# Performance work log

Measured on AMD Instinct MI355X. Metric: run time of the kernel, lower is better.

Reference implementation:

```python
import jax, jax.numpy as jnp
import numpy as np

# Winograd F(4x4, 5x5) transform matrices (input tile 8x8)
AT_NP = np.array([
    [1.0, 1.0, 1.0, 1.0, 1.0, 8.0, 8.0, 0.0],
    [0.0, 1.0, -1.0, 2.0, -2.0, 4.0, -4.0, 0.0],
    [0.0, 1.0, 1.0, 4.0, 4.0, 2.0, 2.0, 0.0],
    [0.0, 1.0, -1.0, 8.0, -8.0, 1.0, -1.0, 1.0]], dtype=np.float32)

BT_NP = np.array([
    [1.0, 0.0, -21.0/4.0, 0.0, 21.0/4.0, 0.0, -1.0, 0.0],
    [0.0, 1.0, 1.0, -17.0/4.0, -17.0/4.0, 1.0, 1.0, 0.0],
    [0.0, -1.0, 1.0, 17.0/4.0, -17.0/4.0, -1.0, 1.0, 0.0],
    [0.0, 0.5, 0.25, -2.5, -1.25, 2.0, 1.0, 0.0],
    [0.0, -0.5, 0.25, 2.5, -1.25, -2.0, 1.0, 0.0],
    [0.0, 2.0, 4.0, -2.5, -5.0, 0.5, 1.0, 0.0],
    [0.0, -2.0, 4.0, 2.5, -5.0, -0.5, 1.0, 0.0],
    [0.0, -1.0, 0.0, 21.0/4.0, 0.0, -21.0/4.0, 0.0, 1.0]], dtype=np.float32)

N, IC, OC, HW = 8, 128, 128, 68  # output spatial = 68-5+1 = 64, tiles 16x16


def setup_inputs() -> dict:
    key = jax.random.key(0)
    k1, k2, k3 = jax.random.split(key, 3)
    x = jax.random.normal(k1, (N, IC, HW, HW), dtype=jnp.float32)
    # weight is stored in the Winograd (transformed) domain: [OC, IC, 8, 8]
    weight = jax.random.normal(k2, (OC, IC, 8, 8), dtype=jnp.float32) * 0.02
    bias = 1.0 + 0.01 * jax.random.normal(k3, (OC,), dtype=jnp.float32)
    return {"x": x, "weight": weight, "bias": bias}


def reference(x, weight, bias):
    BT = jnp.asarray(BT_NP)
    AT = jnp.asarray(AT_NP)
    n, c, H, W = x.shape
    oc = weight.shape[0]
    tH = (H - 8) // 4 + 1
    tW = (W - 8) // 4 + 1
    # extract overlapping 8x8 tiles with stride 4 (torch unfold)
    ih = (jnp.arange(tH) * 4)[:, None] + jnp.arange(8)  # [tH, 8]
    iw = (jnp.arange(tW) * 4)[:, None] + jnp.arange(8)  # [tW, 8]
    tiles = x[:, :, ih, :]            # [n, c, tH, 8, W]
    tiles = tiles[:, :, :, :, iw]     # [n, c, tH, 8, tW, 8]
    tiles = tiles.transpose(0, 1, 2, 4, 3, 5)  # [n, c, tH, tW, 8, 8]
    # input transform: BT @ d @ B
    xt = jnp.einsum('ai,nchwij,bj->nchwab', BT, tiles, BT)
    # channel reduction with elementwise 8x8 multiply (Winograd domain)
    yt = jnp.einsum('nchwab,ocab->nohwab', xt, weight)
    # output transform: AT @ m @ A -> [n, oc, tH, tW, 4, 4]
    y = jnp.einsum('pa,nohwab,qb->nohwpq', AT, yt, AT)
    y = y.transpose(0, 1, 2, 4, 3, 5).reshape(n, oc, tH * 4, tW * 4)
    return y + bias[None, :, None, None]
```

## Files before the change

### kernel.cpp

```cpp
#include <hip/hip_runtime.h>

#define N_    8
#define IC_   128
#define OC_   128
#define HW_   68
#define M_    2048
#define OW_   64

constexpr float BT[8][8] = {
  {1.f, 0.f, -5.25f, 0.f, 5.25f, 0.f, -1.f, 0.f},
  {0.f, 1.f, 1.f, -4.25f, -4.25f, 1.f, 1.f, 0.f},
  {0.f, -1.f, 1.f, 4.25f, -4.25f, -1.f, 1.f, 0.f},
  {0.f, 0.5f, 0.25f, -2.5f, -1.25f, 2.f, 1.f, 0.f},
  {0.f, -0.5f, 0.25f, 2.5f, -1.25f, -2.f, 1.f, 0.f},
  {0.f, 2.f, 4.f, -2.5f, -5.f, 0.5f, 1.f, 0.f},
  {0.f, -2.f, 4.f, 2.5f, -5.f, -0.5f, 1.f, 0.f},
  {0.f, -1.f, 0.f, 5.25f, 0.f, -5.25f, 0.f, 1.f}
};
constexpr float AT[4][8] = {
  {1.f, 1.f, 1.f, 1.f, 1.f, 8.f, 8.f, 0.f},
  {0.f, 1.f, -1.f, 2.f, -2.f, 4.f, -4.f, 0.f},
  {0.f, 1.f, 1.f, 4.f, 4.f, 2.f, 2.f, 0.f},
  {0.f, 1.f, -1.f, 8.f, -8.f, 1.f, -1.f, 1.f}
};

__device__ __forceinline__ float bf2f(unsigned short u) {
  union { unsigned int i; float f; } v; v.i = ((unsigned int)u) << 16; return v.f;
}
__device__ __forceinline__ unsigned short f2bf(float f) {
  union { float f; unsigned int i; } v; v.f = f;
  unsigned int r = v.i + 0x7FFFu + ((v.i >> 16) & 1u);
  return (unsigned short)(r >> 16);
}

typedef __attribute__((ext_vector_type(8))) short short8;
typedef __attribute__((ext_vector_type(4))) float f32x4;

#define K1_CB 16
#define K1_PS 548
__global__ __launch_bounds__(256) void k_input_tf(const float* __restrict__ x,
                                                  unsigned short* __restrict__ xt) {
  const int cg = blockIdx.x, th = blockIdx.y, n = blockIdx.z;
  const int c0 = cg * K1_CB;
  const int h0 = th * 4;
  __shared__ float xs[K1_CB * K1_PS];

  const int tid = threadIdx.x;
  for (int idx = tid; idx < K1_CB * 8 * 17; idx += 256) {
    const int ci = idx / 136;
    const int rem = idx - ci * 136;
    const int r = rem / 17;
    const int f = rem - r * 17;
    const float4 v = *reinterpret_cast<const float4*>(
        x + ((size_t)((n * IC_ + c0 + ci) * HW_ + h0 + r)) * HW_ + f * 4);
    *reinterpret_cast<float4*>(&xs[ci * K1_PS + r * 68 + f * 4]) = v;
  }
  __syncthreads();

  const int cl = tid & 15;
  const int tw = tid >> 4;
  const float* xp = &xs[cl * K1_PS];

  float t1[8][8];
#pragma unroll
  for (int a = 0; a < 8; ++a)
#pragma unroll
    for (int j = 0; j < 8; ++j) t1[a][j] = 0.f;

#pragma unroll
  for (int i = 0; i < 8; ++i) {
    const float4 v0 = *reinterpret_cast<const float4*>(xp + i * 68 + tw * 4);
    const float4 v1 = *reinterpret_cast<const float4*>(xp + i * 68 + tw * 4 + 4);
    const float r[8] = {v0.x, v0.y, v0.z, v0.w, v1.x, v1.y, v1.z, v1.w};
#pragma unroll
    for (int a = 0; a < 8; ++a) {
      const float ba = BT[a][i];
      if (ba != 0.f) {
#pragma unroll
        for (int j = 0; j < 8; ++j) t1[a][j] += ba * r[j];
      }
    }
  }

  const int m = n * 256 + th * 16 + tw;
  const size_t base = (size_t)m * 128 + c0 + cl;
#pragma unroll
  for (int a = 0; a < 8; ++a) {
#pragma unroll
    for (int b = 0; b < 8; ++b) {
      float v = 0.f;
#pragma unroll
      for (int j = 0; j < 8; ++j) {
        const float bb = BT[b][j];
        if (bb != 0.f) v += t1[a][j] * bb;
      }
      xt[(size_t)(a * 8 + b) * (M_ * 128) + base] = f2bf(v);
    }
  }
}

__global__ __launch_bounds__(256) void k_wt(const float* __restrict__ w,
                                            unsigned short* __restrict__ wT) {
  const int idx = blockIdx.x * 256 + threadIdx.x;
  const int c  = idx & 127;
  const int oc = (idx >> 7) & 127;
  const int ab = idx >> 14;
  wT[idx] = f2bf(w[((size_t)oc * IC_ + c) * 64 + ab]);
}

__global__ __launch_bounds__(256) void k_gemm(const unsigned short* __restrict__ xt,
                                              const unsigned short* __restrict__ wT,
                                              unsigned short* __restrict__ yt) {
  const int ab = blockIdx.z;
  const int m0 = blockIdx.x * 64;
  const unsigned short* Ag = xt + (size_t)ab * (M_ * 128);
  const unsigned short* Bg = wT + (size_t)ab * (128 * 128);
  unsigned short* Cg = yt + (size_t)ab * (M_ * 128);

  __shared__ unsigned short As[64 * 128];
  __shared__ unsigned short Bs[128 * 128];

  const int tid = threadIdx.x;
  const int lane = tid & 63;
  const int wv = tid >> 6;

#pragma unroll
  for (int i = 0; i < 4; ++i) {
    const int inst = wv * 4 + i;
    const int r = inst * 4 + (lane >> 4);
    const int j = (lane & 15) ^ (r & 7);
    __builtin_amdgcn_global_load_lds(
        (const __attribute__((address_space(1))) void*)(Ag + (size_t)(m0 + r) * 128 + j * 8),
        (__attribute__((address_space(3))) void*)(As + inst * 512), 16, 0, 0);
  }
#pragma unroll
  for (int i = 0; i < 8; ++i) {
    const int inst = wv * 8 + i;
    const int r = inst * 4 + (lane >> 4);
    const int j = (lane & 15) ^ (r & 7);
    __builtin_amdgcn_global_load_lds(
        (const __attribute__((address_space(1))) void*)(Bg + (size_t)r * 128 + j * 8),
        (__attribute__((address_space(3))) void*)(Bs + inst * 512), 16, 0, 0);
  }
  __syncthreads();

  const int wm = wv >> 1, wn = wv & 1;
  const int m_base = wm * 32;
  const int oc_base = wn * 64;
  const int lr = lane & 15;
  const int lg = lane >> 4;

  f32x4 acc[2][4];
#pragma unroll
  for (int mi = 0; mi < 2; ++mi)
#pragma unroll
    for (int ni = 0; ni < 4; ++ni) acc[mi][ni] = (f32x4){0.f, 0.f, 0.f, 0.f};

#pragma unroll
  for (int kk = 0; kk < 4; ++kk) {
    short8 af[2], bf[4];
#pragma unroll
    for (int mi = 0; mi < 2; ++mi) {
      const int row = m_base + mi * 16 + lr;
      const int chunk = (kk * 4 + lg) ^ (row & 7);
      af[mi] = *reinterpret_cast<const short8*>(&As[row * 128 + chunk * 8]);
    }
#pragma unroll
    for (int ni = 0; ni < 4; ++ni) {
      const int row = oc_base + ni * 16 + lr;
      const int chunk = (kk * 4 + lg) ^ (row & 7);
      bf[ni] = *reinterpret_cast<const short8*>(&Bs[row * 128 + chunk * 8]);
    }
#pragma unroll
    for (int mi = 0; mi < 2; ++mi)
#pragma unroll
      for (int ni = 0; ni < 4; ++ni)
        acc[mi][ni] = __builtin_amdgcn_mfma_f32_16x16x32_bf16(af[mi], bf[ni], acc[mi][ni], 0, 0, 0);
  }

#pragma unroll
  for (int mi = 0; mi < 2; ++mi) {
#pragma unroll
    for (int ni = 0; ni < 4; ++ni) {
#pragma unroll
      for (int j = 0; j < 4; ++j) {
        const int row = m0 + m_base + mi * 16 + lg * 4 + j;
        const int col = oc_base + ni * 16 + lr;
        Cg[(size_t)row * 128 + col] = f2bf(acc[mi][ni][j]);
      }
    }
  }
}

#define K4_PS 260
__global__ __launch_bounds__(512) void k_output_tf(const unsigned short* __restrict__ yt,
                                                   const float* __restrict__ bias,
                                                   float* __restrict__ y) {
  const int og = blockIdx.x, th = blockIdx.y, n = blockIdx.z;
  const int oc0 = og * 32;
  const int tid = threadIdx.x;
  const int ocl = tid & 31;
  const int tw = tid >> 5;
  const int m = n * 256 + th * 16 + tw;

  __shared__ float ys[32 * K4_PS];

  float Y[8][8];
  const size_t rb = (size_t)m * 128 + oc0 + ocl;
#pragma unroll
  for (int a = 0; a < 8; ++a)
#pragma unroll
    for (int b = 0; b < 8; ++b)
      Y[a][b] = bf2f(yt[(size_t)(a * 8 + b) * (M_ * 128) + rb]);

  float t2[4][8];
#pragma unroll
  for (int p = 0; p < 4; ++p)
#pragma unroll
    for (int b = 0; b < 8; ++b) {
      float v = 0.f;
#pragma unroll
      for (int a = 0; a < 8; ++a) {
        const float aa = AT[p][a];
        if (aa != 0.f) v += aa * Y[a][b];
      }
      t2[p][b] = v;
    }

  const float bv = bias[oc0 + ocl];
#pragma unroll
  for (int p = 0; p < 4; ++p) {
    float o[4];
#pragma unroll
    for (int q = 0; q < 4; ++q) {
      float v = 0.f;
#pragma unroll
      for (int b = 0; b < 8; ++b) {
        const float ab_ = AT[q][b];
        if (ab_ != 0.f) v += t2[p][b] * ab_;
      }
      o[q] = v + bv;
    }
    const float4 ov = {o[0], o[1], o[2], o[3]};
    *reinterpret_cast<float4*>(&ys[ocl * K4_PS + p * 64 + tw * 4]) = ov;
  }
  __syncthreads();

#pragma unroll
  for (int it = 0; it < 4; ++it) {
    const int idx = it * 512 + tid;
    const int f = idx & 15;
    const int p = (idx >> 4) & 3;
    const int oo = idx >> 6;
    const float4 v = *reinterpret_cast<const float4*>(&ys[oo * K4_PS + p * 64 + f * 4]);
    *reinterpret_cast<float4*>(
        y + ((size_t)((n * OC_ + oc0 + oo) * OW_) + th * 4 + p) * OW_ + f * 4) = v;
  }
}

extern "C" void kernel_launch(void* const* d_in, const int* in_sizes, int n_in,
                              void* d_out, int out_size, void* d_ws, size_t ws_size,
                              hipStream_t stream) {
  (void)in_sizes; (void)n_in; (void)out_size; (void)ws_size;
  const float* x    = (const float*)d_in[0];
  const float* w    = (const float*)d_in[1];
  const float* bias = (const float*)d_in[2];
  float* y = (float*)d_out;

  char* ws = (char*)d_ws;
  unsigned short* xt = (unsigned short*)ws;
  unsigned short* yt = (unsigned short*)(ws + (size_t)32 * 1024 * 1024);
  unsigned short* wT = (unsigned short*)(ws + (size_t)64 * 1024 * 1024);

  hipLaunchKernelGGL(k_input_tf, dim3(8, 16, 8), dim3(256), 0, stream, x, xt);
  hipLaunchKernelGGL(k_wt, dim3((64 * 128 * 128) / 256), dim3(256), 0, stream, w, wT);
  hipLaunchKernelGGL(k_gemm, dim3(32, 1, 64), dim3(256), 0, stream, xt, wT, yt);
  hipLaunchKernelGGL(k_output_tf, dim3(4, 16, 8), dim3(512), 0, stream, yt, bias, y);
}
```

Before: 120.7 us.

## Fuse batched Winograd GEMM with output transform using multi-stage LDS pipeline

Merges the per-(a,b) batched GEMM and the output-transform kernel into one kernel. Each block computes a 16-tile by 64-channel slab across all 64 Winograd positions and applies the AT transforms in registers, so the bf16 yt intermediate is never written to or read from global memory. Loads for each position are pipelined through a 4-deep LDS ring with explicit vmcnt waits. In exchange, the grid drops to 256 blocks, and the B operand is reloaded once per M block, so weight traffic grows and parallelism is lower.

Measured after the change: 130.8 us. 8.4% more time.

```diff
diff --git a/kernel.cpp b/kernel.cpp
--- a/kernel.cpp
+++ b/kernel.cpp
@@ -108,153 +108,124 @@
   wT[idx] = f2bf(w[((size_t)oc * IC_ + c) * 64 + ab]);
 }
 
-__global__ __launch_bounds__(256) void k_gemm(const unsigned short* __restrict__ xt,
-                                              const unsigned short* __restrict__ wT,
-                                              unsigned short* __restrict__ yt) {
-  const int ab = blockIdx.z;
-  const int m0 = blockIdx.x * 64;
-  const unsigned short* Ag = xt + (size_t)ab * (M_ * 128);
-  const unsigned short* Bg = wT + (size_t)ab * (128 * 128);
-  unsigned short* Cg = yt + (size_t)ab * (M_ * 128);
-
-  __shared__ unsigned short As[64 * 128];
-  __shared__ unsigned short Bs[128 * 128];
+__global__ __launch_bounds__(256) void k_gemm_out(const unsigned short* __restrict__ xt,
+                                                  const unsigned short* __restrict__ wT,
+                                                  const float* __restrict__ bias,
+                                                  float* __restrict__ y) {
+  const int mb = blockIdx.x;
+  const int ob = blockIdx.y;
+  const int m0 = mb * 16;
+  const int oc0 = ob * 64;
+  const int n  = mb >> 4;
+  const int th = mb & 15;
+
+  __shared__ unsigned short As[4][16 * 128];
+  __shared__ unsigned short Bs[4][64 * 128];
+  __shared__ float ys[64 * 68];
 
   const int tid = threadIdx.x;
   const int lane = tid & 63;
   const int wv = tid >> 6;
-
-#pragma unroll
-  for (int i = 0; i < 4; ++i) {
-    const int inst = wv * 4 + i;
-    const int r = inst * 4 + (lane >> 4);
-    const int j = (lane & 15) ^ (r & 7);
-    __builtin_amdgcn_global_load_lds(
-        (const __attribute__((address_space(1))) void*)(Ag + (size_t)(m0 + r) * 128 + j * 8),
-        (__attribute__((address_space(3))) void*)(As + inst * 512), 16, 0, 0);
-  }
-#pragma unroll
-  for (int i = 0; i < 8; ++i) {
-    const int inst = wv * 8 + i;
-    const int r = inst * 4 + (lane >> 4);
-    const int j = (lane & 15) ^ (r & 7);
-    __builtin_amdgcn_global_load_lds(
-        (const __attribute__((address_space(1))) void*)(Bg + (size_t)r * 128 + j * 8),
-        (__attribute__((address_space(3))) void*)(Bs + inst * 512), 16, 0, 0);
-  }
-  __syncthreads();
-
-  const int wm = wv >> 1, wn = wv & 1;
-  const int m_base = wm * 32;
-  const int oc_base = wn * 64;
   const int lr = lane & 15;
   const int lg = lane >> 4;
 
-  f32x4 acc[2][4];
-#pragma unroll
-  for (int mi = 0; mi < 2; ++mi)
-#pragma unroll
-    for (int ni = 0; ni < 4; ++ni) acc[mi][ni] = (f32x4){0.f, 0.f, 0.f, 0.f};
-
-#pragma unroll
-  for (int kk = 0; kk < 4; ++kk) {
-    short8 af[2], bf[4];
-#pragma unroll
-    for (int mi = 0; mi < 2; ++mi) {
-      const int row = m_base + mi * 16 + lr;
-      const int chunk = (kk * 4 + lg) ^ (row & 7);
-      af[mi] = *reinterpret_cast<const short8*>(&As[row * 128 + chunk * 8]);
-    }
-#pragma unroll
-    for (int ni = 0; ni < 4; ++ni) {
-      const int row = oc_base + ni * 16 + lr;
-      const int chunk = (kk * 4 + lg) ^ (row & 7);
-      bf[ni] = *reinterpret_cast<const short8*>(&Bs[row * 128 + chunk * 8]);
-    }
-#pragma unroll
-    for (int mi = 0; mi < 2; ++mi)
-#pragma unroll
-      for (int ni = 0; ni < 4; ++ni)
-        acc[mi][ni] = __builtin_amdgcn_mfma_f32_16x16x32_bf16(af[mi], bf[ni], acc[mi][ni], 0, 0, 0);
-  }
-
-#pragma unroll
-  for (int mi = 0; mi < 2; ++mi) {
-#pragma unroll
-    for (int ni = 0; ni < 4; ++ni) {
+#define STAGE(s_) do {                                                              \
+    const int ab_ = (((s_) & 7) << 3) + ((s_) >> 3);                                \
+    const unsigned short* Ag_ = xt + (size_t)ab_ * (M_ * 128) + (size_t)m0 * 128;   \
+    const unsigned short* Bg_ = wT + (size_t)ab_ * (128 * 128) + (size_t)oc0 * 128; \
+    { const int r_ = wv * 4 + (lane >> 4);                                          \
+      const int j_ = (lane & 15) ^ (r_ & 7);                                        \
+      __builtin_amdgcn_global_load_lds(                                             \
+        (const __attribute__((address_space(1))) void*)(Ag_ + r_ * 128 + j_ * 8),   \
+        (__attribute__((address_space(3))) void*)(&As[(s_) & 3][wv * 512]), 16, 0, 0); } \
+    _Pragma("unroll")                                                               \
+    for (int i_ = 0; i_ < 4; ++i_) {                                                \
+      const int inst_ = wv * 4 + i_;                                                \
+      const int r_ = inst_ * 4 + (lane >> 4);                                       \
+      const int j_ = (lane & 15) ^ (r_ & 7);                                        \
+      __builtin_amdgcn_global_load_lds(                                             \
+        (const __attribute__((address_space(1))) void*)(Bg_ + r_ * 128 + j_ * 8),   \
+        (__attribute__((address_space(3))) void*)(&Bs[(s_) & 3][inst_ * 512]), 16, 0, 0); } \
+  } while (0)
+
+  float y_acc[4][4][4] = {};
+
+  STAGE(0); STAGE(1); STAGE(2);
+
+#pragma unroll
+  for (int b = 0; b < 8; ++b) {
+    float u[4][4];
+#pragma unroll
+    for (int a = 0; a < 8; ++a) {
+      const int s = b * 8 + a;
+      if (s <= 61)      asm volatile("s_waitcnt vmcnt(10)" ::: "memory");
+      else if (s == 62) asm volatile("s_waitcnt vmcnt(5)" ::: "memory");
+      else              asm volatile("s_waitcnt vmcnt(0)" ::: "memory");
+      __builtin_amdgcn_s_barrier();
+      if (s <= 60) STAGE(s + 3);
+
+      const int buf = s & 3;
+      f32x4 cc = (f32x4){0.f, 0.f, 0.f, 0.f};
+#pragma unroll
+      for (int kk = 0; kk < 4; ++kk) {
+        const int arow = lr;
+        const int brow = wv * 16 + lr;
+        const short8 af = *reinterpret_cast<const short8*>(
+            &As[buf][arow * 128 + ((kk * 4 + lg) ^ (arow & 7)) * 8]);
+        const short8 bf = *reinterpret_cast<const short8*>(
+            &Bs[buf][brow * 128 + ((kk * 4 + lg) ^ (brow & 7)) * 8]);
+        cc = __builtin_amdgcn_mfma_f32_16x16x32_bf16(af, bf, cc, 0, 0, 0);
+      }
+
 #pragma unroll
       for (int j = 0; j < 4; ++j) {
-        const int row = m0 + m_base + mi * 16 + lg * 4 + j;
-        const int col = oc_base + ni * 16 + lr;
-        Cg[(size_t)row * 128 + col] = f2bf(acc[mi][ni][j]);
-      }
-    }
-  }
-}
-
-#define K4_PS 260
-__global__ __launch_bounds__(512) void k_output_tf(const unsigned short* __restrict__ yt,
-                                                   const float* __restrict__ bias,
-                                                   float* __restrict__ y) {
-  const int og = blockIdx.x, th = blockIdx.y, n = blockIdx.z;
-  const int oc0 = og * 32;
-  const int tid = threadIdx.x;
-  const int ocl = tid & 31;
-  const int tw = tid >> 5;
-  const int m = n * 256 + th * 16 + tw;
-
-  __shared__ float ys[32 * K4_PS];
-
-  float Y[8][8];
-  const size_t rb = (size_t)m * 128 + oc0 + ocl;
-#pragma unroll
-  for (int a = 0; a < 8; ++a)
-#pragma unroll
-    for (int b = 0; b < 8; ++b)
-      Y[a][b] = bf2f(yt[(size_t)(a * 8 + b) * (M_ * 128) + rb]);
-
-  float t2[4][8];
-#pragma unroll
-  for (int p = 0; p < 4; ++p)
-#pragma unroll
-    for (int b = 0; b < 8; ++b) {
-      float v = 0.f;
-#pragma unroll
-      for (int a = 0; a < 8; ++a) {
-        const float aa = AT[p][a];
-        if (aa != 0.f) v += aa * Y[a][b];
-      }
-      t2[p][b] = v;
-    }
-
-  const float bv = bias[oc0 + ocl];
+        const float cv = cc[j];
+#pragma unroll
+        for (int p = 0; p < 4; ++p) {
+          const float w_ = AT[p][a];
+          if (a == 0)           u[j][p] = w_ * cv;
+          else if (w_ != 0.f)   u[j][p] += w_ * cv;
+        }
+      }
+      if (a == 7) {
+#pragma unroll
+        for (int q = 0; q < 4; ++q) {
+          const float wq = AT[q][b];
+          if (wq != 0.f) {
+#pragma unroll
+            for (int j = 0; j < 4; ++j)
+#pragma unroll
+              for (int p = 0; p < 4; ++p)
+                y_acc[j][p][q] += wq * u[j][p];
+          }
+        }
+      }
+    }
+  }
+#undef STAGE
+
+  const int oc_loc = wv * 16 + lr;
+  const float bv = bias[oc0 + oc_loc];
 #pragma unroll
   for (int p = 0; p < 4; ++p) {
-    float o[4];
-#pragma unroll
-    for (int q = 0; q < 4; ++q) {
-      float v = 0.f;
-#pragma unroll
-      for (int b = 0; b < 8; ++b) {
-        const float ab_ = AT[q][b];
-        if (ab_ != 0.f) v += t2[p][b] * ab_;
-      }
-      o[q] = v + bv;
-    }
-    const float4 ov = {o[0], o[1], o[2], o[3]};
-    *reinterpret_cast<float4*>(&ys[ocl * K4_PS + p * 64 + tw * 4]) = ov;
-  }
-  __syncthreads();
-
-#pragma unroll
-  for (int it = 0; it < 4; ++it) {
-    const int idx = it * 512 + tid;
-    const int f = idx & 15;
-    const int p = (idx >> 4) & 3;
-    const int oo = idx >> 6;
-    const float4 v = *reinterpret_cast<const float4*>(&ys[oo * K4_PS + p * 64 + f * 4]);
-    *reinterpret_cast<float4*>(
-        y + ((size_t)((n * OC_ + oc0 + oo) * OW_) + th * 4 + p) * OW_ + f * 4) = v;
+#pragma unroll
+    for (int j = 0; j < 4; ++j) {
+      const int m_loc = lg * 4 + j;
+      const float4 v = {y_acc[j][p][0] + bv, y_acc[j][p][1] + bv,
+                        y_acc[j][p][2] + bv, y_acc[j][p][3] + bv};
+      *reinterpret_cast<float4*>(&ys[oc_loc * 68 + m_loc * 4]) = v;
+    }
+    __syncthreads();
+#pragma unroll
+    for (int it = 0; it < 4; ++it) {
+      const int idx = it * 256 + tid;
+      const int row = idx >> 4;
+      const int f = idx & 15;
+      const float4 v = *reinterpret_cast<const float4*>(&ys[row * 68 + f * 4]);
+      *reinterpret_cast<float4*>(
+          y + (((size_t)(n * OC_ + oc0 + row) * OW_) + th * 4 + p) * OW_ + f * 4) = v;
+    }
+    __syncthreads();
   }
 }
 
@@ -269,11 +240,9 @@
 
   char* ws = (char*)d_ws;
   unsigned short* xt = (unsigned short*)ws;
-  unsigned short* yt = (unsigned short*)(ws + (size_t)32 * 1024 * 1024);
-  unsigned short* wT = (unsigned short*)(ws + (size_t)64 * 1024 * 1024);
+  unsigned short* wT = (unsigned short*)(ws + (size_t)32 * 1024 * 1024);
 
   hipLaunchKernelGGL(k_input_tf, dim3(8, 16, 8), dim3(256), 0, stream, x, xt);
   hipLaunchKernelGGL(k_wt, dim3((64 * 128 * 128) / 256), dim3(256), 0, stream, w, wT);
-  hipLaunchKernelGGL(k_gemm, dim3(32, 1, 64), dim3(256), 0, stream, xt, wT, yt);
-  hipLaunchKernelGGL(k_output_tf, dim3(4, 16, 8), dim3(512), 0, stream, yt, bias, y);
-}
+  hipLaunchKernelGGL(k_gemm_out, dim3(128, 2), dim3(256), 0, stream, xt, wT, bias, y);
+}
```
